# Performance work log

Hardware: AMD Instinct MI355X
Metric: run time of the kernel (lower is better)

The kernel has to match this reference:

```python
import jax, jax.numpy as jnp
import numpy as np

N = 100_000        # nodes
E = 1_600_000      # edges
F_IN = 128         # n_node_f == out_dim (residual)
F_EDGE = 16        # n_edge_f
HEADS = 4
C = 32             # out_dim // heads
NEG_SLOPE = 0.2


def setup_inputs() -> dict:
    key = jax.random.key(0)
    ks = jax.random.split(key, 10)
    x = jax.random.normal(ks[0], (N, F_IN), jnp.float32)
    edge_index = jax.random.randint(ks[1], (2, E), 0, N, dtype=jnp.int32)
    edge_attr = jax.random.normal(ks[2], (E, F_EDGE), jnp.float32)
    u = jax.random.normal(ks[3], (1, 64), jnp.float32)
    batch = jnp.zeros((N,), jnp.int32)
    # GATv2Conv parameters (glorot-ish scales)
    Wl = jax.random.normal(ks[4], (HEADS * C, F_IN), jnp.float32) / np.sqrt(F_IN).astype(np.float32)
    bl = jnp.zeros((HEADS * C,), jnp.float32)
    Wr = jax.random.normal(ks[5], (HEADS * C, F_IN), jnp.float32) / np.sqrt(F_IN).astype(np.float32)
    br = jnp.zeros((HEADS * C,), jnp.float32)
    We = jax.random.normal(ks[6], (HEADS * C, F_EDGE), jnp.float32) / np.sqrt(F_EDGE).astype(np.float32)
    att = jax.random.normal(ks[7], (HEADS, C), jnp.float32) / np.sqrt(C).astype(np.float32)
    bias = jnp.zeros((HEADS * C,), jnp.float32)
    return {"x": x, "edge_index": edge_index, "edge_attr": edge_attr, "u": u,
            "batch": batch, "Wl": Wl, "bl": bl, "Wr": Wr, "br": br,
            "We": We, "att": att, "bias": bias}


def _gatv2(x, edge_index, edge_attr, Wl, bl, Wr, br, We, att, bias):
    src, dst = edge_index[0], edge_index[1]
    # add_self_loops with fill_value='mean': self-loop edge_attr = mean of
    # incoming edge features per target node
    deg = jax.ops.segment_sum(jnp.ones((E,), x.dtype), dst, num_segments=N)
    ea_mean = jax.ops.segment_sum(edge_attr, dst, num_segments=N) / jnp.maximum(deg, 1.0)[:, None]
    loop = jnp.arange(N, dtype=src.dtype)
    src2 = jnp.concatenate([src, loop])            # [E+N]
    dst2 = jnp.concatenate([dst, loop])            # [E+N]
    ea2 = jnp.concatenate([edge_attr, ea_mean], 0)  # [E+N, F_EDGE]

    x_l = (x @ Wl.T + bl).reshape(N, HEADS, C)     # source projection
    x_r = (x @ Wr.T + br).reshape(N, HEADS, C)     # target projection
    e = (ea2 @ We.T).reshape(-1, HEADS, C)          # edge projection (no bias)

    # GATv2 attention: score = att . leaky_relu(x_l[j] + x_r[i] + e)
    act = jax.nn.leaky_relu(x_l[src2] + x_r[dst2] + e, NEG_SLOPE)  # [E+N, H, C]
    logits = jnp.einsum('ehc,hc->eh', act, att)                     # [E+N, H]

    # segment softmax over incoming edges of each destination node
    m = jax.ops.segment_max(logits, dst2, num_segments=N)           # [N, H]
    p = jnp.exp(logits - m[dst2])
    denom = jax.ops.segment_sum(p, dst2, num_segments=N)            # [N, H]
    alpha = p / denom[dst2]                                         # [E+N, H]

    out = jax.ops.segment_sum(alpha[:, :, None] * x_l[src2], dst2, num_segments=N)
    return out.reshape(N, HEADS * C) + bias


def reference(x, edge_index, edge_attr, u, batch, Wl, bl, Wr, br, We, att, bias):
    out = jax.nn.relu(_gatv2(x, edge_index, edge_attr, Wl, bl, Wr, br, We, att, bias))
    return out + x  # residuals=True
```

## Files before the change

### kernel.cpp

```cpp
#include <hip/hip_runtime.h>
#include <hip/hip_bf16.h>
#include <math.h>

#define N_NODES 100000
#define N_EDGES 1600000
#define F_IN 128
#define F_EDGE 16
#define HC 128
#define NB_SCAN 98

typedef unsigned int uint;

__device__ __forceinline__ float bf_lo(uint u) { return __uint_as_float(u << 16); }
__device__ __forceinline__ float bf_hi(uint u) { return __uint_as_float(u & 0xffff0000u); }
__device__ __forceinline__ uint f2bfbits(float f) {
    union { __hip_bfloat16 h; unsigned short u; } cv;
    cv.h = __float2bfloat16(f);
    return (uint)cv.u;
}
__device__ __forceinline__ uint pack_bf2(float lo, float hi) {
    return f2bfbits(lo) | (f2bfbits(hi) << 16);
}

#if defined(__has_builtin)
#if __has_builtin(__builtin_amdgcn_fdot2_f32_bf16)
#define HAVE_DOT2_BF16 1
#endif
#endif

#ifdef HAVE_DOT2_BF16
typedef __attribute__((ext_vector_type(2))) __bf16 bf16x2_t;
__device__ __forceinline__ float dot2bf(uint a, uint b, float c) {
    return __builtin_amdgcn_fdot2_f32_bf16(
        __builtin_bit_cast(bf16x2_t, a), __builtin_bit_cast(bf16x2_t, b), c, false);
}
#else
__device__ __forceinline__ float dot2bf(uint a, uint b, float c) {
    return fmaf(bf_lo(a), bf_lo(b), fmaf(bf_hi(a), bf_hi(b), c));
}
#endif

__global__ __launch_bounds__(256) void proj_kernel(
    const float* __restrict__ x,
    const float* __restrict__ Wl, const float* __restrict__ bl,
    const float* __restrict__ Wr, const float* __restrict__ br,
    unsigned short* __restrict__ xlb, unsigned short* __restrict__ xrb)
{
    __shared__ uint2 xs[64 * 32];
    __shared__ uint2 ws[64 * 32];

    int bx = blockIdx.x;
    int rb = bx >> 2;
    int cb = bx & 3;
    int row0 = rb * 64;
    int col0 = (cb & 1) * 64;
    const float* W    = (cb < 2) ? Wl : Wr;
    const float* bias = (cb < 2) ? bl : br;
    unsigned short* outb = (cb < 2) ? xlb : xrb;

    int tid = threadIdx.x;

    #pragma unroll
    for (int i = 0; i < 8; ++i) {
        int f  = tid + 256 * i;
        int r  = f >> 5;
        int u  = f & 31;
        int gr = row0 + r;
        float4 v = make_float4(0.f, 0.f, 0.f, 0.f);
        if (gr < N_NODES) v = ((const float4*)(x + (size_t)gr * F_IN))[u];
        uint2 pv; pv.x = pack_bf2(v.x, v.y); pv.y = pack_bf2(v.z, v.w);
        xs[r * 32 + (u ^ (r & 31))] = pv;
    }
    #pragma unroll
    for (int i = 0; i < 8; ++i) {
        int f  = tid + 256 * i;
        int r  = f >> 5;
        int u  = f & 31;
        float4 v = ((const float4*)(W + (size_t)(col0 + r) * F_IN))[u];
        uint2 pv; pv.x = pack_bf2(v.x, v.y); pv.y = pack_bf2(v.z, v.w);
        ws[r * 32 + (u ^ (r & 31))] = pv;
    }
    __syncthreads();

    int tx = tid & 15, ty = tid >> 4;
    float acc[4][4];
    #pragma unroll
    for (int i = 0; i < 4; ++i)
        #pragma unroll
        for (int j = 0; j < 4; ++j) acc[i][j] = 0.f;

    for (int u = 0; u < 32; ++u) {
        uint2 a[4], b[4];
        #pragma unroll
        for (int i = 0; i < 4; ++i) {
            int r = ty + 16 * i;
            a[i] = xs[r * 32 + (u ^ (r & 31))];
        }
        #pragma unroll
        for (int j = 0; j < 4; ++j) {
            int r = tx + 16 * j;
            b[j] = ws[r * 32 + (u ^ (r & 31))];
        }
        #pragma unroll
        for (int i = 0; i < 4; ++i)
            #pragma unroll
            for (int j = 0; j < 4; ++j) {
                acc[i][j] = dot2bf(a[i].x, b[j].x, acc[i][j]);
                acc[i][j] = dot2bf(a[i].y, b[j].y, acc[i][j]);
            }
    }

    #pragma unroll
    for (int i = 0; i < 4; ++i) {
        int gr = row0 + ty + 16 * i;
        if (gr >= N_NODES) continue;
        #pragma unroll
        for (int j = 0; j < 4; ++j) {
            int c = col0 + tx + 16 * j;
            float v = acc[i][j] + bias[c];
            outb[(size_t)gr * HC + c] = (unsigned short)f2bfbits(v);
        }
    }
}

__global__ void count_kernel(const int* __restrict__ dst, int* __restrict__ deg)
{
    int e = blockIdx.x * blockDim.x + threadIdx.x;
    if (e < N_EDGES) atomicAdd(&deg[dst[e]], 1);
}

__global__ __launch_bounds__(1024) void scan1_kernel(
    const int* __restrict__ deg, int* __restrict__ row_start, int* __restrict__ bsum)
{
    __shared__ int sm[1024];
    int t = threadIdx.x;
    int i = blockIdx.x * 1024 + t;
    int v = (i < N_NODES) ? deg[i] : 0;
    sm[t] = v;
    __syncthreads();
    for (int off = 1; off < 1024; off <<= 1) {
        int o = (t >= off) ? sm[t - off] : 0;
        __syncthreads();
        sm[t] += o;
        __syncthreads();
    }
    if (i < N_NODES) row_start[i] = sm[t] - v;
    if (t == 1023) bsum[blockIdx.x] = sm[1023];
}

__global__ __launch_bounds__(128) void scan2_kernel(
    const int* __restrict__ bsum, int* __restrict__ boff)
{
    __shared__ int sm[128];
    int t = threadIdx.x;
    int v = (t < NB_SCAN) ? bsum[t] : 0;
    sm[t] = v;
    __syncthreads();
    for (int off = 1; off < 128; off <<= 1) {
        int o = (t >= off) ? sm[t - off] : 0;
        __syncthreads();
        sm[t] += o;
        __syncthreads();
    }
    if (t < NB_SCAN) boff[t] = sm[t] - v;
}

__global__ __launch_bounds__(1024) void scan3_kernel(
    int* __restrict__ row_start, const int* __restrict__ boff, int* __restrict__ cursor)
{
    int i = blockIdx.x * 1024 + threadIdx.x;
    if (i < N_NODES) {
        int r = row_start[i] + boff[blockIdx.x];
        row_start[i] = r;
        cursor[i] = r;
    }
    if (i == 0) row_start[N_NODES] = N_EDGES;
}

__global__ void scatter_kernel(
    const int* __restrict__ src, const int* __restrict__ dst,
    const float* __restrict__ edge_attr,
    int* __restrict__ cursor, int* __restrict__ csr_src, uint4* __restrict__ csr_ea)
{
    int e = blockIdx.x * blockDim.x + threadIdx.x;
    if (e < N_EDGES) {
        int d   = dst[e];
        int pos = atomicAdd(&cursor[d], 1);
        csr_src[pos] = src[e];
        const float4* ep = (const float4*)(edge_attr + (size_t)e * F_EDGE);
        float4 t0 = ep[0], t1 = ep[1], t2 = ep[2], t3 = ep[3];
        uint4 a, b;
        a.x = pack_bf2(t0.x, t0.y);  a.y = pack_bf2(t0.z, t0.w);
        a.z = pack_bf2(t1.x, t1.y);  a.w = pack_bf2(t1.z, t1.w);
        b.x = pack_bf2(t2.x, t2.y);  b.y = pack_bf2(t2.z, t2.w);
        b.z = pack_bf2(t3.x, t3.y);  b.w = pack_bf2(t3.z, t3.w);
        csr_ea[2 * (size_t)pos]     = a;
        csr_ea[2 * (size_t)pos + 1] = b;
    }
}

__global__ __launch_bounds__(256, 4) void node_kernel(
    const float* __restrict__ x, const unsigned short* __restrict__ xlb,
    const unsigned short* __restrict__ xrb,
    const int* __restrict__ row_start, const int* __restrict__ csr_src,
    const uint* __restrict__ ea_w,
    const float* __restrict__ We, const float* __restrict__ att,
    const float* __restrict__ bias, float* __restrict__ out)
{
    int wid  = threadIdx.x >> 6;
    uint lane = threadIdx.x & 63;
    int node = blockIdx.x * 4 + wid;
    if (node >= N_NODES) return;

    int c0 = 2 * lane, c1 = 2 * lane + 1;

    uint wpA[8], wpB[8];
    {
        const float4* wa = (const float4*)(We + (size_t)c0 * F_EDGE);
        const float4* wb = (const float4*)(We + (size_t)c1 * F_EDGE);
        #pragma unroll
        for (int q = 0; q < 4; ++q) {
            float4 va = wa[q], vb = wb[q];
            wpA[2*q]   = pack_bf2(va.x, va.y);
            wpA[2*q+1] = pack_bf2(va.z, va.w);
            wpB[2*q]   = pack_bf2(vb.x, vb.y);
            wpB[2*q+1] = pack_bf2(vb.z, vb.w);
        }
    }
    float attA = att[c0], attB = att[c1];
    float attA6 = 0.6f * attA, attA4 = 0.4f * attA;
    float attB6 = 0.6f * attB, attB4 = 0.4f * attB;
    uint xru = ((const uint*)xrb)[(uint)node * 64u + lane];
    float xrA = bf_lo(xru), xrB = bf_hi(xru);

    int rs = row_start[node], re = row_start[node + 1];
    int deg = re - rs;

    const uint* xl32 = (const uint*)xlb;

    float d = 0.f, accA = 0.f, accB = 0.f;
    float eAs = 0.f, eBs = 0.f;

    auto edge_core = [&](float eA, float eB, uint g) {
        eAs += eA; eBs += eB;
        float xlA = bf_lo(g), xlB = bf_hi(g);
        float sA = eA + xlA;
        float sB = eB + xlB;
        float p = attA6 * sA;
        p = fmaf(attA4, fabsf(sA), p);
        p = fmaf(attB6, sB, p);
        p = fmaf(attB4, fabsf(sB), p);
        p += __shfl_xor(p, 1);
        p += __shfl_xor(p, 2);
        p += __shfl_xor(p, 4);
        p += __shfl_xor(p, 8);
        float w = __expf(p);
        d += w;
        accA = fmaf(w, xlA, accA);
        accB = fmaf(w, xlB, accB);
    };

    int ngrp = deg >> 3;
    if (ngrp > 0) {
        int sA8 = 0, sB8 = 0;
        uint wA = 0, wB = 0;
        uint gA[8], gB[8];

        auto LOADW = [&](int jb, int& s8, uint& w) {
            s8 = csr_src[(uint)jb + (lane >> 3)];
            w  = ea_w[(uint)jb * 8u + lane];
        };
        auto GATHER = [&](int s8, uint g[8]) {
            #pragma unroll
            for (int k = 0; k < 8; ++k) {
                uint s = (uint)__builtin_amdgcn_readlane(s8, 8 * k);
                g[k] = xl32[s * 64u + lane];
            }
        };
        auto COMP = [&](uint w, const uint g[8]) {
            #pragma unroll
            for (int k = 0; k < 8; ++k) {
                float eA = xrA, eB = xrB;
                #pragma unroll
                for (int j = 0; j < 8; ++j) {
                    uint ew = (uint)__builtin_amdgcn_readlane((int)w, 8 * k + j);
                    eA = dot2bf(ew, wpA[j], eA);
                    eB = dot2bf(ew, wpB[j], eB);
                }
                edge_core(eA, eB, g[k]);
            }
        };

        LOADW(rs, sA8, wA);
        if (ngrp > 1) LOADW(rs + 8, sB8, wB);
        GATHER(sA8, gA);
        for (int gq = 0; gq < ngrp; gq += 2) {
            bool hasB = (gq + 1 < ngrp);
            if (hasB) GATHER(sB8, gB);
            int sN = 0; uint wN = 0;
            if (gq + 2 < ngrp) LOADW(rs + 8 * (gq + 2), sN, wN);
            COMP(wA, gA);
            sA8 = sN; wA = wN;
            if (hasB) {
                if (gq + 2 < ngrp) GATHER(sA8, gA);
                int sM = 0; uint wM = 0;
                if (gq + 3 < ngrp) LOADW(rs + 8 * (gq + 3), sM, wM);
                COMP(wB, gB);
                sB8 = sM; wB = wM;
            }
        }
    }
    for (int j = rs + (ngrp << 3); j < re; ++j) {
        uint s = (uint)csr_src[j];
        uint g = xl32[s * 64u + lane];
        const uint4* ep = (const uint4*)(ea_w + (uint)j * 8u);
        uint4 a = ep[0], b = ep[1];
        uint ea[8] = {a.x, a.y, a.z, a.w, b.x, b.y, b.z, b.w};
        float eA = xrA, eB = xrB;
        #pragma unroll
        for (int k = 0; k < 8; ++k) {
            eA = dot2bf(ea[k], wpA[k], eA);
            eB = dot2bf(ea[k], wpB[k], eB);
        }
        edge_core(eA, eB, g);
    }

    {
        uint g = xl32[(uint)node * 64u + lane];
        float xlA = bf_lo(g), xlB = bf_hi(g);
        float eA, eB;
        if (deg > 0) {
            float inv = 1.f / (float)deg;
            eA = eAs * inv; eB = eBs * inv;
        } else {
            eA = xrA; eB = xrB;
        }
        float sA = eA + xlA;
        float sB = eB + xlB;
        float p = attA6 * sA;
        p = fmaf(attA4, fabsf(sA), p);
        p = fmaf(attB6, sB, p);
        p = fmaf(attB4, fabsf(sB), p);
        p += __shfl_xor(p, 1);
        p += __shfl_xor(p, 2);
        p += __shfl_xor(p, 4);
        p += __shfl_xor(p, 8);
        float w = __expf(p);
        d += w;
        accA = fmaf(w, xlA, accA);
        accB = fmaf(w, xlB, accB);
    }

    float invd = 1.f / d;
    float oA = accA * invd + bias[c0];
    float oB = accB * invd + bias[c1];
    float2 xv = *(const float2*)(x + (uint)node * HC + c0);
    float2 o;
    o.x = fmaxf(oA, 0.f) + xv.x;
    o.y = fmaxf(oB, 0.f) + xv.y;
    *(float2*)(out + (uint)node * HC + c0) = o;
}

extern "C" void kernel_launch(void* const* d_in, const int* in_sizes, int n_in,
                              void* d_out, int out_size, void* d_ws, size_t ws_size,
                              hipStream_t stream)
{
    const float* x         = (const float*)d_in[0];
    const int*   ei        = (const int*)d_in[1];
    const float* edge_attr = (const float*)d_in[2];
    const float* Wl   = (const float*)d_in[5];
    const float* bl   = (const float*)d_in[6];
    const float* Wr   = (const float*)d_in[7];
    const float* br   = (const float*)d_in[8];
    const float* We   = (const float*)d_in[9];
    const float* att  = (const float*)d_in[10];
    const float* bias = (const float*)d_in[11];
    float* out = (float*)d_out;

    const int* src = ei;
    const int* dst = ei + N_EDGES;

    char* p = (char*)d_ws;
    auto alloc = [&](size_t bytes) {
        void* r = (void*)p;
        p += (bytes + 255) & ~(size_t)255;
        return r;
    };
    unsigned short* xlb = (unsigned short*)alloc((size_t)N_NODES * HC * sizeof(unsigned short));
    unsigned short* xrb = (unsigned short*)alloc((size_t)N_NODES * HC * sizeof(unsigned short));
    int* deg        = (int*)alloc((size_t)N_NODES * sizeof(int));
    int* row_start  = (int*)alloc((size_t)(N_NODES + 1) * sizeof(int));
    int* cursor     = (int*)alloc((size_t)N_NODES * sizeof(int));
    int* csr_src    = (int*)alloc((size_t)N_EDGES * sizeof(int));
    uint4* csr_ea   = (uint4*)alloc((size_t)N_EDGES * 2 * sizeof(uint4));
    int* bsum       = (int*)alloc(256 * sizeof(int));
    int* boff       = (int*)alloc(256 * sizeof(int));

    hipMemsetAsync(deg, 0, (size_t)N_NODES * sizeof(int), stream);

    {
        int rblocks = (N_NODES + 63) / 64;
        proj_kernel<<<rblocks * 4, 256, 0, stream>>>(x, Wl, bl, Wr, br, xlb, xrb);
    }
    count_kernel<<<(N_EDGES + 255) / 256, 256, 0, stream>>>(dst, deg);
    scan1_kernel<<<NB_SCAN, 1024, 0, stream>>>(deg, row_start, bsum);
    scan2_kernel<<<1, 128, 0, stream>>>(bsum, boff);
    scan3_kernel<<<NB_SCAN, 1024, 0, stream>>>(row_start, boff, cursor);
    scatter_kernel<<<(N_EDGES + 255) / 256, 256, 0, stream>>>(src, dst, edge_attr, cursor, csr_src, csr_ea);
    node_kernel<<<(N_NODES + 3) / 4, 256, 0, stream>>>(
        x, xlb, xrb, row_start, csr_src, (const uint*)csr_ea, We, att, bias, out);
}
```

Before: 501.1 us.

## Use MFMA bf16 for node projections and fuse conversion with degree counting

Replaces the LDS-tiled dot2 projection GEMM with an MFMA 16x16x32 bf16 kernel that reads pre-converted bf16 x and weights straight from global memory. A new kernel fuses the fp32-to-bf16 conversion of x and the weights into the degree-count pass, relying on N*F_IN/8 equalling N_EDGES so one thread per edge also converts one 8-element chunk. This adds a bf16 copy of x in workspace and an extra round trip through memory, in exchange for using matrix cores and dropping a kernel launch.

Result: faster. 474.9 us (-5.2%).

```diff
diff --git a/kernel.cpp b/kernel.cpp
--- a/kernel.cpp
+++ b/kernel.cpp
@@ -10,6 +10,8 @@
 #define NB_SCAN 98
 
 typedef unsigned int uint;
+typedef __attribute__((ext_vector_type(8))) short short8;
+typedef __attribute__((ext_vector_type(4))) float f32x4;
 
 __device__ __forceinline__ float bf_lo(uint u) { return __uint_as_float(u << 16); }
 __device__ __forceinline__ float bf_hi(uint u) { return __uint_as_float(u & 0xffff0000u); }
@@ -40,93 +42,88 @@
 }
 #endif
 
-__global__ __launch_bounds__(256) void proj_kernel(
+__global__ void cvt_count_kernel(
     const float* __restrict__ x,
-    const float* __restrict__ Wl, const float* __restrict__ bl,
-    const float* __restrict__ Wr, const float* __restrict__ br,
+    const float* __restrict__ Wl, const float* __restrict__ Wr,
+    const int* __restrict__ dst, int* __restrict__ deg,
+    uint4* __restrict__ xb4, uint4* __restrict__ wb4)
+{
+    int t = blockIdx.x * 256 + threadIdx.x;
+    if (t < N_EDGES) {
+        atomicAdd(&deg[dst[t]], 1);
+        const float4* xp = (const float4*)x + (size_t)t * 2;
+        float4 v0 = xp[0], v1 = xp[1];
+        uint4 o;
+        o.x = pack_bf2(v0.x, v0.y); o.y = pack_bf2(v0.z, v0.w);
+        o.z = pack_bf2(v1.x, v1.y); o.w = pack_bf2(v1.z, v1.w);
+        xb4[t] = o;
+    }
+    if (t < 4096) {
+        const float* W = (t < 2048) ? Wl : Wr;
+        const float4* wp = (const float4*)W + (size_t)(t & 2047) * 2;
+        float4 v0 = wp[0], v1 = wp[1];
+        uint4 o;
+        o.x = pack_bf2(v0.x, v0.y); o.y = pack_bf2(v0.z, v0.w);
+        o.z = pack_bf2(v1.x, v1.y); o.w = pack_bf2(v1.z, v1.w);
+        wb4[t] = o;
+    }
+}
+
+__global__ __launch_bounds__(256) void proj_mfma_kernel(
+    const uint4* __restrict__ xb4, const uint4* __restrict__ wb4,
+    const float* __restrict__ bl, const float* __restrict__ br,
     unsigned short* __restrict__ xlb, unsigned short* __restrict__ xrb)
 {
-    __shared__ uint2 xs[64 * 32];
-    __shared__ uint2 ws[64 * 32];
-
-    int bx = blockIdx.x;
-    int rb = bx >> 2;
-    int cb = bx & 3;
-    int row0 = rb * 64;
-    int col0 = (cb & 1) * 64;
-    const float* W    = (cb < 2) ? Wl : Wr;
-    const float* bias = (cb < 2) ? bl : br;
-    unsigned short* outb = (cb < 2) ? xlb : xrb;
-
-    int tid = threadIdx.x;
-
-    #pragma unroll
-    for (int i = 0; i < 8; ++i) {
-        int f  = tid + 256 * i;
-        int r  = f >> 5;
-        int u  = f & 31;
-        int gr = row0 + r;
-        float4 v = make_float4(0.f, 0.f, 0.f, 0.f);
-        if (gr < N_NODES) v = ((const float4*)(x + (size_t)gr * F_IN))[u];
-        uint2 pv; pv.x = pack_bf2(v.x, v.y); pv.y = pack_bf2(v.z, v.w);
-        xs[r * 32 + (u ^ (r & 31))] = pv;
-    }
-    #pragma unroll
-    for (int i = 0; i < 8; ++i) {
-        int f  = tid + 256 * i;
-        int r  = f >> 5;
-        int u  = f & 31;
-        float4 v = ((const float4*)(W + (size_t)(col0 + r) * F_IN))[u];
-        uint2 pv; pv.x = pack_bf2(v.x, v.y); pv.y = pack_bf2(v.z, v.w);
-        ws[r * 32 + (u ^ (r & 31))] = pv;
-    }
-    __syncthreads();
-
-    int tx = tid & 15, ty = tid >> 4;
-    float acc[4][4];
+    int w  = threadIdx.x >> 6;
+    int l  = threadIdx.x & 63;
+    int rl = l & 15;
+    int kg = l >> 4;
+    int row0 = blockIdx.x * 64;
+    int col0 = w * 64;
+
+    f32x4 acc[4][4];
     #pragma unroll
     for (int i = 0; i < 4; ++i)
         #pragma unroll
-        for (int j = 0; j < 4; ++j) acc[i][j] = 0.f;
-
-    for (int u = 0; u < 32; ++u) {
-        uint2 a[4], b[4];
-        #pragma unroll
-        for (int i = 0; i < 4; ++i) {
-            int r = ty + 16 * i;
-            a[i] = xs[r * 32 + (u ^ (r & 31))];
-        }
-        #pragma unroll
-        for (int j = 0; j < 4; ++j) {
-            int r = tx + 16 * j;
-            b[j] = ws[r * 32 + (u ^ (r & 31))];
-        }
-        #pragma unroll
-        for (int i = 0; i < 4; ++i)
+        for (int j = 0; j < 4; ++j) acc[i][j] = (f32x4){0.f, 0.f, 0.f, 0.f};
+
+    #pragma unroll
+    for (int kk = 0; kk < 4; ++kk) {
+        short8 a[4];
+        #pragma unroll
+        for (int rt = 0; rt < 4; ++rt) {
+            int row = row0 + rt * 16 + rl;
+            if (row >= N_NODES) row = N_NODES - 1;
+            a[rt] = __builtin_bit_cast(short8, xb4[(uint)row * 16u + kk * 4 + kg]);
+        }
+        #pragma unroll
+        for (int ct = 0; ct < 4; ++ct) {
+            int ch = col0 + ct * 16 + rl;
+            short8 b = __builtin_bit_cast(short8, wb4[(uint)ch * 16u + kk * 4 + kg]);
             #pragma unroll
-            for (int j = 0; j < 4; ++j) {
-                acc[i][j] = dot2bf(a[i].x, b[j].x, acc[i][j]);
-                acc[i][j] = dot2bf(a[i].y, b[j].y, acc[i][j]);
+            for (int rt = 0; rt < 4; ++rt)
+                acc[rt][ct] = __builtin_amdgcn_mfma_f32_16x16x32_bf16(
+                    a[rt], b, acc[rt][ct], 0, 0, 0);
+        }
+    }
+
+    #pragma unroll
+    for (int ct = 0; ct < 4; ++ct) {
+        int ch = col0 + ct * 16 + rl;
+        float bs = (ch < HC) ? bl[ch] : br[ch - HC];
+        unsigned short* outp = (ch < HC) ? xlb : xrb;
+        uint chm = (uint)(ch & 127);
+        #pragma unroll
+        for (int rt = 0; rt < 4; ++rt) {
+            #pragma unroll
+            for (int r = 0; r < 4; ++r) {
+                int row = row0 + rt * 16 + 4 * kg + r;
+                if (row < N_NODES)
+                    outp[(uint)row * 128u + chm] =
+                        (unsigned short)f2bfbits(acc[rt][ct][r] + bs);
             }
-    }
-
-    #pragma unroll
-    for (int i = 0; i < 4; ++i) {
-        int gr = row0 + ty + 16 * i;
-        if (gr >= N_NODES) continue;
-        #pragma unroll
-        for (int j = 0; j < 4; ++j) {
-            int c = col0 + tx + 16 * j;
-            float v = acc[i][j] + bias[c];
-            outb[(size_t)gr * HC + c] = (unsigned short)f2bfbits(v);
-        }
-    }
-}
-
-__global__ void count_kernel(const int* __restrict__ dst, int* __restrict__ deg)
-{
-    int e = blockIdx.x * blockDim.x + threadIdx.x;
-    if (e < N_EDGES) atomicAdd(&deg[dst[e]], 1);
+        }
+    }
 }
 
 __global__ __launch_bounds__(1024) void scan1_kernel(
@@ -388,6 +385,8 @@
     };
     unsigned short* xlb = (unsigned short*)alloc((size_t)N_NODES * HC * sizeof(unsigned short));
     unsigned short* xrb = (unsigned short*)alloc((size_t)N_NODES * HC * sizeof(unsigned short));
+    uint4* xb4      = (uint4*)alloc((size_t)N_NODES * HC * sizeof(unsigned short));
+    uint4* wb4      = (uint4*)alloc((size_t)2 * HC * F_IN * sizeof(unsigned short));
     int* deg        = (int*)alloc((size_t)N_NODES * sizeof(int));
     int* row_start  = (int*)alloc((size_t)(N_NODES + 1) * sizeof(int));
     int* cursor     = (int*)alloc((size_t)N_NODES * sizeof(int));
@@ -398,11 +397,8 @@
 
     hipMemsetAsync(deg, 0, (size_t)N_NODES * sizeof(int), stream);
 
-    {
-        int rblocks = (N_NODES + 63) / 64;
-        proj_kernel<<<rblocks * 4, 256, 0, stream>>>(x, Wl, bl, Wr, br, xlb, xrb);
-    }
-    count_kernel<<<(N_EDGES + 255) / 256, 256, 0, stream>>>(dst, deg);
+    cvt_count_kernel<<<N_EDGES / 256, 256, 0, stream>>>(x, Wl, Wr, dst, deg, xb4, wb4);
+    proj_mfma_kernel<<<(N_NODES + 63) / 64, 256, 0, stream>>>(xb4, wb4, bl, br, xlb, xrb);
     scan1_kernel<<<NB_SCAN, 1024, 0, stream>>>(deg, row_start, bsum);
     scan2_kernel<<<1, 128, 0, stream>>>(bsum, boff);
     scan3_kernel<<<NB_SCAN, 1024, 0, stream>>>(row_start, boff, cursor);
```
